# Kernel tuning notes

Measured on AMD Instinct MI355X. Metric: run time of the kernel, lower is better.

The kernel has to match this reference:

```python
import jax, jax.numpy as jnp
import numpy as np

NUM_SPARSE = 26
VOCAB = 100000
EMB = 64
B = 2048
DENSE = 13
NUM_FEA = NUM_SPARSE + 1  # 26 embeddings + bottom-MLP output


def _xavier(key, shape):
    fan_in, fan_out = shape[0], shape[1]
    lim = jnp.sqrt(6.0 / (fan_in + fan_out))
    return jax.random.uniform(key, shape, jnp.float32, -lim, lim)


def setup_inputs() -> dict:
    key = jax.random.key(0)
    ks = jax.random.split(key, 20)
    inp = {
        "dense": jax.random.normal(ks[0], (B, DENSE), jnp.float32),
        "cat_idx": jax.random.randint(ks[1], (B, NUM_SPARSE), 0, VOCAB, jnp.int32),
        # stacked EmbeddingBag tables (all same vocab -> one [26, V, 64] tensor)
        "tables": _xavier(ks[2], (VOCAB, EMB))[None] * jnp.ones((NUM_SPARSE, 1, 1), jnp.float32) * 0
                  + jax.random.normal(ks[3], (NUM_SPARSE, VOCAB, EMB), jnp.float32) * 0.01,
        # bottom MLP: 13 -> 512 -> 256 -> 64
        "bw0": _xavier(ks[4], (DENSE, 512)), "bb0": jnp.zeros((512,), jnp.float32),
        "bw1": _xavier(ks[5], (512, 256)),   "bb1": jnp.zeros((256,), jnp.float32),
        "bw2": _xavier(ks[6], (256, EMB)),   "bb2": jnp.zeros((EMB,), jnp.float32),
        # top MLP: 415 -> 1024 -> 512 -> 256 -> 1
        "tw0": _xavier(ks[7], (EMB + NUM_FEA * (NUM_FEA - 1) // 2, 1024)), "tb0": jnp.zeros((1024,), jnp.float32),
        "tw1": _xavier(ks[8], (1024, 512)),  "tb1": jnp.zeros((512,), jnp.float32),
        "tw2": _xavier(ks[9], (512, 256)),   "tb2": jnp.zeros((256,), jnp.float32),
        "tw3": _xavier(ks[10], (256, 1)),    "tb3": jnp.zeros((1,), jnp.float32),
    }
    return inp


def reference(dense, cat_idx, tables, bw0, bb0, bw1, bb1, bw2, bb2,
              tw0, tb0, tw1, tb1, tw2, tb2, tw3, tb3):
    # bottom MLP on dense features -> [B, EMB]
    h = jax.nn.relu(dense @ bw0 + bb0)
    h = jax.nn.relu(h @ bw1 + bb1)
    bot = jax.nn.relu(h @ bw2 + bb2)

    # EmbeddingBag (single index per bag, sum mode == plain gather): [B, 26, EMB]
    feat_ids = jnp.arange(NUM_SPARSE)[None, :]  # [1, 26]
    emb = tables[feat_ids, cat_idx]             # [B, 26, EMB]

    # dot interaction: batched Gram matrix then lower-triangular gather
    T = jnp.concatenate([bot[:, None, :], emb], axis=1)  # [B, 27, EMB]
    Z = jnp.einsum("bif,bjf->bij", T, T)                  # [B, 27, 27]
    li, lj = np.tril_indices(NUM_FEA, k=-1)               # 351 pairs
    Zflat = Z[:, li, lj]                                  # [B, 351]

    R = jnp.concatenate([bot, Zflat], axis=1)             # [B, 415]

    # top MLP
    r = jax.nn.relu(R @ tw0 + tb0)
    r = jax.nn.relu(r @ tw1 + tb1)
    r = jax.nn.relu(r @ tw2 + tb2)
    out = jax.nn.sigmoid(r @ tw3 + tb3)                   # [B, 1]
    return out
```

## Files before the change

### kernel.cpp

```cpp
#include <hip/hip_runtime.h>
#include <hip/hip_bf16.h>


#define BATCH 2048
#define VOCAB 100000
#define EMB 64
#define NSPARSE 26
#define NFEA 27
#define NPAIR 351
#define RLD 416

typedef __attribute__((ext_vector_type(8))) __bf16 bf16x8;
typedef __attribute__((ext_vector_type(4))) float f32x4;
typedef __hip_bfloat16 bf16;

#define GLOAD16(g, l)                                                          \
    __builtin_amdgcn_global_load_lds(                                          \
        (const __attribute__((address_space(1))) unsigned int*)(g),            \
        (__attribute__((address_space(3))) unsigned int*)(l), 16, 0, 0)

__global__ __launch_bounds__(256) void gemm_bf16(
    const bf16* __restrict__ A,
    const bf16* __restrict__ Wt,
    const float* __restrict__ bias,
    bf16* __restrict__ C,
    int M, int N, int K, int ldC)
{
    __shared__ __align__(16) bf16 As[64 * 32];
    __shared__ __align__(16) bf16 Bs[64 * 32];

    const int t   = threadIdx.x;
    const int nbn = N >> 6;
    const int bm  = blockIdx.x / nbn;
    const int bn  = blockIdx.x % nbn;
    const int row0 = bm << 6, n0 = bn << 6;

    const int wid  = t >> 6, lane = t & 63;
    const int wr   = wid >> 1, wc = wid & 1;
    const int lr   = lane & 15;
    const int q    = lane >> 4;

    const int srow = t >> 2, sslot = t & 3;
    const int sswz = sslot ^ ((srow >> 1) & 3);
    const char* gA = (const char*)(A  + (size_t)(row0 + srow) * K) + sswz * 16;
    const char* gB = (const char*)(Wt + (size_t)(n0   + srow) * K) + sswz * 16;
    char* lA = (char*)As + t * 16;
    char* lB = (char*)Bs + t * 16;

    f32x4 acc[2][2] = {};

    const int arow0 = wr * 32 + lr;
    const int brow0 = wc * 32 + lr;

    for (int k0 = 0; k0 < K; k0 += 32) {
        GLOAD16(gA + (size_t)k0 * 2, lA);
        GLOAD16(gB + (size_t)k0 * 2, lB);
        __syncthreads();

        bf16x8 af[2], bf[2];
#pragma unroll
        for (int m = 0; m < 2; ++m) {
            const int r = arow0 + 16 * m;
            af[m] = *(const bf16x8*)((const char*)As + r * 64 +
                                     ((q ^ ((r >> 1) & 3)) << 4));
        }
#pragma unroll
        for (int n = 0; n < 2; ++n) {
            const int r = brow0 + 16 * n;
            bf[n] = *(const bf16x8*)((const char*)Bs + r * 64 +
                                     ((q ^ ((r >> 1) & 3)) << 4));
        }
#pragma unroll
        for (int m = 0; m < 2; ++m)
#pragma unroll
            for (int n = 0; n < 2; ++n)
                acc[m][n] = __builtin_amdgcn_mfma_f32_16x16x32_bf16(
                    af[m], bf[n], acc[m][n], 0, 0, 0);
        __syncthreads();
    }

#pragma unroll
    for (int n = 0; n < 2; ++n) {
        const int col = n0 + wc * 32 + 16 * n + lr;
        const float bv = bias[col];
#pragma unroll
        for (int m = 0; m < 2; ++m) {
#pragma unroll
            for (int i = 0; i < 4; ++i) {
                const int row = row0 + wr * 32 + 16 * m + q * 4 + i;
                float v = acc[m][n][i] + bv;
                v = fmaxf(v, 0.f);
                C[(size_t)row * ldC + col] = __float2bfloat16(v);
            }
        }
    }
}

struct WConvArgs {
    const float* src[6];
    bf16*        dst[6];
    int K[6], N[6], Kp[6], t0[7];
};

__global__ __launch_bounds__(256) void wconv_kernel(WConvArgs a)
{
    __shared__ float Ts[32][33];
    int w = 0;
    while (w < 5 && (int)blockIdx.x >= a.t0[w + 1]) ++w;
    const int rel = blockIdx.x - a.t0[w];
    const int K = a.K[w], N = a.N[w], Kp = a.Kp[w];
    const int nbn = N >> 5;
    const int tk = rel / nbn, tn = rel % nbn;
    const int tx = threadIdx.x & 31, ty = threadIdx.x >> 5;

    const float* src = a.src[w];
    bf16* dst = a.dst[w];

#pragma unroll
    for (int rr = 0; rr < 4; ++rr) {
        const int k = tk * 32 + ty + rr * 8;
        const int n = tn * 32 + tx;
        Ts[ty + rr * 8][tx] = (k < K) ? src[(size_t)k * N + n] : 0.f;
    }
    __syncthreads();
#pragma unroll
    for (int rr = 0; rr < 4; ++rr) {
        const int n = tn * 32 + ty + rr * 8;
        const int kp = tk * 32 + tx;
        dst[(size_t)n * Kp + kp] = __float2bfloat16(Ts[tx][ty + rr * 8]);
    }
}

__global__ __launch_bounds__(256) void densepad_kernel(
    const float* __restrict__ dense, bf16* __restrict__ out)
{
    const int i = blockIdx.x * 256 + threadIdx.x;
    const int b = i >> 5, c = i & 31;
    out[i] = (c < 13) ? __float2bfloat16(dense[b * 13 + c]) : __float2bfloat16(0.f);
}

__global__ __launch_bounds__(256) void interact_kernel(
    const int* __restrict__ cat_idx, const float* __restrict__ tables,
    bf16* __restrict__ R)
{
    __shared__ float T[NFEA][EMB + 1];

    const int b    = blockIdx.x;
    const int t    = threadIdx.x;
    const int g    = t >> 6;
    const int lane = t & 63;
    bf16* Rrow = R + (size_t)b * RLD;

    for (int f = g; f < NFEA; f += 4) {
        if (f == 0) {
            T[0][lane] = __bfloat162float(Rrow[lane]);
        } else {
            const int j   = f - 1;
            const int idx = cat_idx[b * NSPARSE + j];
            T[f][lane] = tables[((size_t)j * VOCAB + idx) * EMB + lane];
        }
    }
    __syncthreads();

    if (t == 0) Rrow[415] = __float2bfloat16(0.f);

    for (int p = t; p < NPAIR; p += 256) {
        int i = (int)((1.0f + sqrtf(1.0f + 8.0f * (float)p)) * 0.5f);
        while (i * (i - 1) / 2 > p) --i;
        while ((i + 1) * i / 2 <= p) ++i;
        const int j = p - i * (i - 1) / 2;
        float s = 0.f;
#pragma unroll 16
        for (int k = 0; k < EMB; ++k) s += T[i][k] * T[j][k];
        Rrow[EMB + p] = __float2bfloat16(s);
    }
}

__global__ __launch_bounds__(256) void top3_kernel(
    const bf16* __restrict__ A, const float* __restrict__ w,
    const float* __restrict__ bias, float* __restrict__ out)
{
    const int gid  = blockIdx.x * 256 + threadIdx.x;
    const int row  = gid >> 6;
    const int lane = gid & 63;

    const bf16* arow = A + (size_t)row * 256;
    float s = 0.f;
#pragma unroll
    for (int k = lane; k < 256; k += 64)
        s += __bfloat162float(arow[k]) * w[k];
#pragma unroll
    for (int off = 32; off; off >>= 1) s += __shfl_down(s, off);
    if (lane == 0) out[row] = 1.f / (1.f + expf(-(s + bias[0])));
}

extern "C" void kernel_launch(void* const* d_in, const int* in_sizes, int n_in,
                              void* d_out, int out_size, void* d_ws, size_t ws_size,
                              hipStream_t stream)
{
    const float* dense   = (const float*)d_in[0];
    const int*   cat_idx = (const int*)  d_in[1];
    const float* tables  = (const float*)d_in[2];
    const float* bw0 = (const float*)d_in[3];
    const float* bb0 = (const float*)d_in[4];
    const float* bw1 = (const float*)d_in[5];
    const float* bb1 = (const float*)d_in[6];
    const float* bw2 = (const float*)d_in[7];
    const float* bb2 = (const float*)d_in[8];
    const float* tw0 = (const float*)d_in[9];
    const float* tb0 = (const float*)d_in[10];
    const float* tw1 = (const float*)d_in[11];
    const float* tb1 = (const float*)d_in[12];
    const float* tw2 = (const float*)d_in[13];
    const float* tb2 = (const float*)d_in[14];
    const float* tw3 = (const float*)d_in[15];
    const float* tb3 = (const float*)d_in[16];

    bf16* p = (bf16*)d_ws;
    bf16* dense_bf = p; p += (size_t)BATCH * 32;
    bf16* h0   = p; p += (size_t)BATCH * 512;
    bf16* h1   = p; p += (size_t)BATCH * 256;
    bf16* R    = p; p += (size_t)BATCH * RLD;
    bf16* r0   = p; p += (size_t)BATCH * 1024;
    bf16* r1   = p; p += (size_t)BATCH * 512;
    bf16* r2   = p; p += (size_t)BATCH * 256;
    bf16* bw0t = p; p += 512 * 32;
    bf16* bw1t = p; p += 256 * 512;
    bf16* bw2t = p; p += 64 * 256;
    bf16* tw0t = p; p += 1024 * RLD;
    bf16* tw1t = p; p += 512 * 1024;
    bf16* tw2t = p; p += 256 * 512;
    float* out = (float*)d_out;

    WConvArgs wa;
    wa.src[0] = bw0;  wa.dst[0] = bw0t; wa.K[0] = 13;   wa.N[0] = 512;  wa.Kp[0] = 32;
    wa.src[1] = bw1;  wa.dst[1] = bw1t; wa.K[1] = 512;  wa.N[1] = 256;  wa.Kp[1] = 512;
    wa.src[2] = bw2;  wa.dst[2] = bw2t; wa.K[2] = 256;  wa.N[2] = 64;   wa.Kp[2] = 256;
    wa.src[3] = tw0;  wa.dst[3] = tw0t; wa.K[3] = 415;  wa.N[3] = 1024; wa.Kp[3] = RLD;
    wa.src[4] = tw1;  wa.dst[4] = tw1t; wa.K[4] = 1024; wa.N[4] = 512;  wa.Kp[4] = 1024;
    wa.src[5] = tw2;  wa.dst[5] = tw2t; wa.K[5] = 512;  wa.N[5] = 256;  wa.Kp[5] = 512;
    int tiles = 0;
    for (int w = 0; w < 6; ++w) {
        wa.t0[w] = tiles;
        tiles += (wa.Kp[w] >> 5) * (wa.N[w] >> 5);
    }
    wa.t0[6] = tiles;

    wconv_kernel<<<tiles, 256, 0, stream>>>(wa);
    densepad_kernel<<<(BATCH * 32) / 256, 256, 0, stream>>>(dense, dense_bf);

    gemm_bf16<<<(BATCH / 64) * (512 / 64), 256, 0, stream>>>(
        dense_bf, bw0t, bb0, h0, BATCH, 512, 32, 512);
    gemm_bf16<<<(BATCH / 64) * (256 / 64), 256, 0, stream>>>(
        h0, bw1t, bb1, h1, BATCH, 256, 512, 256);
    gemm_bf16<<<(BATCH / 64) * (64 / 64), 256, 0, stream>>>(
        h1, bw2t, bb2, R, BATCH, 64, 256, RLD);

    interact_kernel<<<BATCH, 256, 0, stream>>>(cat_idx, tables, R);

    gemm_bf16<<<(BATCH / 64) * (1024 / 64), 256, 0, stream>>>(
        R, tw0t, tb0, r0, BATCH, 1024, RLD, 1024);
    gemm_bf16<<<(BATCH / 64) * (512 / 64), 256, 0, stream>>>(
        r0, tw1t, tb1, r1, BATCH, 512, 1024, 512);
    gemm_bf16<<<(BATCH / 64) * (256 / 64), 256, 0, stream>>>(
        r1, tw2t, tb2, r2, BATCH, 256, 512, 256);
    top3_kernel<<<BATCH / 4, 256, 0, stream>>>(r2, tw3, tb3, out);
}
```

Before: 72.73 us.

## Fuse entire DLRM forward into one persistent-per-16-rows megakernel

Replaces the chain of densepad, six tiled GEMM launches, the interaction kernel and the final dot kernel with a single kernel where each block owns 16 batch rows and keeps every activation in LDS. Weights are streamed straight from global memory into MFMA operands with no LDS staging. The Gram matrix is now computed with MFMA instead of scalar loops, and the last layer plus sigmoid is folded into the tw2 epilogue. This removes launch overhead and the global round-trips of the intermediate activations. In exchange only 128 blocks run, so each block re-reads all weights from L2, occupancy is low, and the weight loads are not coalesced through shared memory.

New measurement: 120.2 us. 1.65x slower.

```diff
diff --git a/kernel.cpp b/kernel.cpp
--- a/kernel.cpp
+++ b/kernel.cpp
@@ -4,97 +4,12 @@
 
 #define BATCH 2048
 #define VOCAB 100000
-#define EMB 64
-#define NSPARSE 26
-#define NFEA 27
-#define NPAIR 351
-#define RLD 416
 
 typedef __attribute__((ext_vector_type(8))) __bf16 bf16x8;
 typedef __attribute__((ext_vector_type(4))) float f32x4;
 typedef __hip_bfloat16 bf16;
 
-#define GLOAD16(g, l)                                                          \
-    __builtin_amdgcn_global_load_lds(                                          \
-        (const __attribute__((address_space(1))) unsigned int*)(g),            \
-        (__attribute__((address_space(3))) unsigned int*)(l), 16, 0, 0)
-
-__global__ __launch_bounds__(256) void gemm_bf16(
-    const bf16* __restrict__ A,
-    const bf16* __restrict__ Wt,
-    const float* __restrict__ bias,
-    bf16* __restrict__ C,
-    int M, int N, int K, int ldC)
-{
-    __shared__ __align__(16) bf16 As[64 * 32];
-    __shared__ __align__(16) bf16 Bs[64 * 32];
-
-    const int t   = threadIdx.x;
-    const int nbn = N >> 6;
-    const int bm  = blockIdx.x / nbn;
-    const int bn  = blockIdx.x % nbn;
-    const int row0 = bm << 6, n0 = bn << 6;
-
-    const int wid  = t >> 6, lane = t & 63;
-    const int wr   = wid >> 1, wc = wid & 1;
-    const int lr   = lane & 15;
-    const int q    = lane >> 4;
-
-    const int srow = t >> 2, sslot = t & 3;
-    const int sswz = sslot ^ ((srow >> 1) & 3);
-    const char* gA = (const char*)(A  + (size_t)(row0 + srow) * K) + sswz * 16;
-    const char* gB = (const char*)(Wt + (size_t)(n0   + srow) * K) + sswz * 16;
-    char* lA = (char*)As + t * 16;
-    char* lB = (char*)Bs + t * 16;
-
-    f32x4 acc[2][2] = {};
-
-    const int arow0 = wr * 32 + lr;
-    const int brow0 = wc * 32 + lr;
-
-    for (int k0 = 0; k0 < K; k0 += 32) {
-        GLOAD16(gA + (size_t)k0 * 2, lA);
-        GLOAD16(gB + (size_t)k0 * 2, lB);
-        __syncthreads();
-
-        bf16x8 af[2], bf[2];
-#pragma unroll
-        for (int m = 0; m < 2; ++m) {
-            const int r = arow0 + 16 * m;
-            af[m] = *(const bf16x8*)((const char*)As + r * 64 +
-                                     ((q ^ ((r >> 1) & 3)) << 4));
-        }
-#pragma unroll
-        for (int n = 0; n < 2; ++n) {
-            const int r = brow0 + 16 * n;
-            bf[n] = *(const bf16x8*)((const char*)Bs + r * 64 +
-                                     ((q ^ ((r >> 1) & 3)) << 4));
-        }
-#pragma unroll
-        for (int m = 0; m < 2; ++m)
-#pragma unroll
-            for (int n = 0; n < 2; ++n)
-                acc[m][n] = __builtin_amdgcn_mfma_f32_16x16x32_bf16(
-                    af[m], bf[n], acc[m][n], 0, 0, 0);
-        __syncthreads();
-    }
-
-#pragma unroll
-    for (int n = 0; n < 2; ++n) {
-        const int col = n0 + wc * 32 + 16 * n + lr;
-        const float bv = bias[col];
-#pragma unroll
-        for (int m = 0; m < 2; ++m) {
-#pragma unroll
-            for (int i = 0; i < 4; ++i) {
-                const int row = row0 + wr * 32 + 16 * m + q * 4 + i;
-                float v = acc[m][n][i] + bv;
-                v = fmaxf(v, 0.f);
-                C[(size_t)row * ldC + col] = __float2bfloat16(v);
-            }
-        }
-    }
-}
+#define MFMA __builtin_amdgcn_mfma_f32_16x16x32_bf16
 
 struct WConvArgs {
     const float* src[6];
@@ -131,67 +46,194 @@
     }
 }
 
-__global__ __launch_bounds__(256) void densepad_kernel(
-    const float* __restrict__ dense, bf16* __restrict__ out)
-{
-    const int i = blockIdx.x * 256 + threadIdx.x;
-    const int b = i >> 5, c = i & 31;
-    out[i] = (c < 13) ? __float2bfloat16(dense[b * 13 + c]) : __float2bfloat16(0.f);
-}
-
-__global__ __launch_bounds__(256) void interact_kernel(
-    const int* __restrict__ cat_idx, const float* __restrict__ tables,
-    bf16* __restrict__ R)
-{
-    __shared__ float T[NFEA][EMB + 1];
-
-    const int b    = blockIdx.x;
-    const int t    = threadIdx.x;
-    const int g    = t >> 6;
-    const int lane = t & 63;
-    bf16* Rrow = R + (size_t)b * RLD;
-
-    for (int f = g; f < NFEA; f += 4) {
-        if (f == 0) {
-            T[0][lane] = __bfloat162float(Rrow[lane]);
-        } else {
-            const int j   = f - 1;
-            const int idx = cat_idx[b * NSPARSE + j];
-            T[f][lane] = tables[((size_t)j * VOCAB + idx) * EMB + lane];
-        }
-    }
-    __syncthreads();
-
-    if (t == 0) Rrow[415] = __float2bfloat16(0.f);
-
-    for (int p = t; p < NPAIR; p += 256) {
-        int i = (int)((1.0f + sqrtf(1.0f + 8.0f * (float)p)) * 0.5f);
-        while (i * (i - 1) / 2 > p) --i;
-        while ((i + 1) * i / 2 <= p) ++i;
-        const int j = p - i * (i - 1) / 2;
-        float s = 0.f;
-#pragma unroll 16
-        for (int k = 0; k < EMB; ++k) s += T[i][k] * T[j][k];
-        Rrow[EMB + p] = __float2bfloat16(s);
-    }
-}
-
-__global__ __launch_bounds__(256) void top3_kernel(
-    const bf16* __restrict__ A, const float* __restrict__ w,
-    const float* __restrict__ bias, float* __restrict__ out)
-{
-    const int gid  = blockIdx.x * 256 + threadIdx.x;
-    const int row  = gid >> 6;
-    const int lane = gid & 63;
-
-    const bf16* arow = A + (size_t)row * 256;
-    float s = 0.f;
-#pragma unroll
-    for (int k = lane; k < 256; k += 64)
-        s += __bfloat162float(arow[k]) * w[k];
-#pragma unroll
-    for (int off = 32; off; off >>= 1) s += __shfl_down(s, off);
-    if (lane == 0) out[row] = 1.f / (1.f + expf(-(s + bias[0])));
+template<int KSTEPS, int NREP>
+__device__ __forceinline__ void layer(
+    const bf16* actL, int strideA,
+    const bf16* __restrict__ Wt, const float* __restrict__ bias,
+    bf16* outL, int strideO,
+    int wid, int lr, int q)
+{
+    constexpr int K = KSTEPS * 32;
+    const int n0 = wid * NREP * 16;
+
+    const bf16* wp[NREP];
+#pragma unroll
+    for (int n = 0; n < NREP; ++n)
+        wp[n] = Wt + (size_t)(n0 + n * 16 + lr) * K + q * 8;
+    const bf16* ap = actL + lr * strideA + q * 8;
+
+    f32x4 acc[NREP] = {};
+#pragma unroll 4
+    for (int ks = 0; ks < KSTEPS; ++ks) {
+        const bf16x8 af = *(const bf16x8*)(ap + ks * 32);
+#pragma unroll
+        for (int n = 0; n < NREP; ++n) {
+            const bf16x8 bv = *(const bf16x8*)(wp[n] + ks * 32);
+            acc[n] = MFMA(af, bv, acc[n], 0, 0, 0);
+        }
+    }
+
+#pragma unroll
+    for (int n = 0; n < NREP; ++n) {
+        const int col = n0 + n * 16 + lr;
+        const float bv = bias[col];
+#pragma unroll
+        for (int i = 0; i < 4; ++i) {
+            float v = fmaxf(acc[n][i] + bv, 0.f);
+            outL[(q * 4 + i) * strideO + col] = __float2bfloat16(v);
+        }
+    }
+}
+
+__global__ __launch_bounds__(256, 1) void mega(
+    const float* __restrict__ dense, const int* __restrict__ cat,
+    const float* __restrict__ tables,
+    const bf16* __restrict__ bw0t, const float* __restrict__ bb0,
+    const bf16* __restrict__ bw1t, const float* __restrict__ bb1,
+    const bf16* __restrict__ bw2t, const float* __restrict__ bb2,
+    const bf16* __restrict__ tw0t, const float* __restrict__ tb0,
+    const bf16* __restrict__ tw1t, const float* __restrict__ tb1,
+    const bf16* __restrict__ tw2t, const float* __restrict__ tb2,
+    const float* __restrict__ tw3, const float* __restrict__ tb3,
+    float* __restrict__ out)
+{
+    __shared__ __align__(16) bf16 T[16 * 32 * 72];
+    __shared__ __align__(16) bf16 bufA[16 * 264];
+    __shared__ __align__(16) bf16 bufB[16 * 520];
+    __shared__ float rsum[4][16];
+
+    const int t   = threadIdx.x;
+    const int b0  = blockIdx.x * 16;
+    const int wid = t >> 6, lane = t & 63;
+    const int lr  = lane & 15, q = lane >> 4;
+
+    for (int i = t; i < 16 * 32; i += 256) {
+        const int r = i >> 5, c = i & 31;
+        const float v = (c < 13) ? dense[(size_t)(b0 + r) * 13 + c] : 0.f;
+        bufA[r * 40 + c] = __float2bfloat16(v);
+    }
+    __syncthreads();
+
+    layer<1, 8>(bufA, 40, bw0t, bb0, bufB, 520, wid, lr, q);
+    __syncthreads();
+
+    layer<16, 4>(bufB, 520, bw1t, bb1, bufA, 264, wid, lr, q);
+    __syncthreads();
+
+    for (int task = t; task < 416 * 16; task += 256) {
+        const int g = task >> 4, c4 = task & 15;
+        const int r = g / 26, j = g - r * 26;
+        const int idx = cat[(b0 + r) * 26 + j];
+        const float4 v =
+            *(const float4*)&tables[((size_t)j * VOCAB + idx) * 64 + c4 * 4];
+        union { bf16 h[4]; uint2 u; } pk;
+        pk.h[0] = __float2bfloat16(v.x); pk.h[1] = __float2bfloat16(v.y);
+        pk.h[2] = __float2bfloat16(v.z); pk.h[3] = __float2bfloat16(v.w);
+        *(uint2*)&T[(r * 32 + 1 + j) * 72 + c4 * 4] = pk.u;
+    }
+
+    layer<8, 1>(bufA, 264, bw2t, bb2, T, 32 * 72, wid, lr, q);
+
+    for (int i = t; i < 16 * 33; i += 256) {
+        const int r = i / 33, c = i % 33;
+        bufB[r * 456 + 415 + c] = __float2bfloat16(0.f);
+    }
+    __syncthreads();
+
+    for (int i = t; i < 16 * 64; i += 256) {
+        const int r = i >> 6, c = i & 63;
+        bufB[r * 456 + c] = T[r * (32 * 72) + c];
+    }
+
+    {
+#pragma unroll
+        for (int rr = 0; rr < 4; ++rr) {
+            const int r = wid * 4 + rr;
+            const bf16* Tr = T + r * (32 * 72);
+            f32x4 g00 = {}, g10 = {}, g11 = {};
+#pragma unroll
+            for (int ks = 0; ks < 2; ++ks) {
+                const bf16x8 a0 = *(const bf16x8*)(Tr + lr * 72 + ks * 32 + q * 8);
+                const bf16x8 a1 = *(const bf16x8*)(Tr + (16 + lr) * 72 + ks * 32 + q * 8);
+                g00 = MFMA(a0, a0, g00, 0, 0, 0);
+                g10 = MFMA(a1, a0, g10, 0, 0, 0);
+                g11 = MFMA(a1, a1, g11, 0, 0, 0);
+            }
+#pragma unroll
+            for (int i = 0; i < 4; ++i) {
+                {   const int row = q * 4 + i, col = lr;
+                    if (col < row) {
+                        const int p = row * (row - 1) / 2 + col;
+                        bufB[r * 456 + 64 + p] = __float2bfloat16(g00[i]);
+                    } }
+                {   const int row = 16 + q * 4 + i, col = lr;
+                    if (row < 27) {
+                        const int p = row * (row - 1) / 2 + col;
+                        bufB[r * 456 + 64 + p] = __float2bfloat16(g10[i]);
+                    } }
+                {   const int row = 16 + q * 4 + i, col = 16 + lr;
+                    if (row < 27 && col < row) {
+                        const int p = row * (row - 1) / 2 + col;
+                        bufB[r * 456 + 64 + p] = __float2bfloat16(g11[i]);
+                    } }
+            }
+        }
+    }
+    __syncthreads();
+
+    bf16* r0 = T;
+    layer<14, 16>(bufB, 456, tw0t, tb0, r0, 1032, wid, lr, q);
+    __syncthreads();
+
+    layer<32, 8>(r0, 1032, tw1t, tb1, bufB, 520, wid, lr, q);
+    __syncthreads();
+
+    {
+        constexpr int KST = 16, NR = 4;
+        constexpr int K = 512;
+        const int n0 = wid * 64;
+        const bf16* wp[NR];
+#pragma unroll
+        for (int n = 0; n < NR; ++n)
+            wp[n] = tw2t + (size_t)(n0 + n * 16 + lr) * K + q * 8;
+        const bf16* ap = bufB + lr * 520 + q * 8;
+
+        f32x4 acc[NR] = {};
+#pragma unroll 4
+        for (int ks = 0; ks < KST; ++ks) {
+            const bf16x8 af = *(const bf16x8*)(ap + ks * 32);
+#pragma unroll
+            for (int n = 0; n < NR; ++n)
+                acc[n] = MFMA(af, *(const bf16x8*)(wp[n] + ks * 32), acc[n], 0, 0, 0);
+        }
+
+        float s[4] = {0.f, 0.f, 0.f, 0.f};
+#pragma unroll
+        for (int n = 0; n < NR; ++n) {
+            const int col = n0 + n * 16 + lr;
+            const float bv = tb2[col];
+            const float wv = tw3[col];
+#pragma unroll
+            for (int i = 0; i < 4; ++i)
+                s[i] += fmaxf(acc[n][i] + bv, 0.f) * wv;
+        }
+#pragma unroll
+        for (int i = 0; i < 4; ++i) {
+            s[i] += __shfl_xor(s[i], 1);
+            s[i] += __shfl_xor(s[i], 2);
+            s[i] += __shfl_xor(s[i], 4);
+            s[i] += __shfl_xor(s[i], 8);
+        }
+        if (lr == 0) {
+#pragma unroll
+            for (int i = 0; i < 4; ++i) rsum[wid][q * 4 + i] = s[i];
+        }
+        __syncthreads();
+        if (t < 16) {
+            const float tot = rsum[0][t] + rsum[1][t] + rsum[2][t] + rsum[3][t];
+            out[b0 + t] = 1.f / (1.f + expf(-(tot + tb3[0])));
+        }
+    }
 }
 
 extern "C" void kernel_launch(void* const* d_in, const int* in_sizes, int n_in,
@@ -217,17 +259,10 @@
     const float* tb3 = (const float*)d_in[16];
 
     bf16* p = (bf16*)d_ws;
-    bf16* dense_bf = p; p += (size_t)BATCH * 32;
-    bf16* h0   = p; p += (size_t)BATCH * 512;
-    bf16* h1   = p; p += (size_t)BATCH * 256;
-    bf16* R    = p; p += (size_t)BATCH * RLD;
-    bf16* r0   = p; p += (size_t)BATCH * 1024;
-    bf16* r1   = p; p += (size_t)BATCH * 512;
-    bf16* r2   = p; p += (size_t)BATCH * 256;
     bf16* bw0t = p; p += 512 * 32;
     bf16* bw1t = p; p += 256 * 512;
     bf16* bw2t = p; p += 64 * 256;
-    bf16* tw0t = p; p += 1024 * RLD;
+    bf16* tw0t = p; p += 1024 * 448;
     bf16* tw1t = p; p += 512 * 1024;
     bf16* tw2t = p; p += 256 * 512;
     float* out = (float*)d_out;
@@ -236,7 +271,7 @@
     wa.src[0] = bw0;  wa.dst[0] = bw0t; wa.K[0] = 13;   wa.N[0] = 512;  wa.Kp[0] = 32;
     wa.src[1] = bw1;  wa.dst[1] = bw1t; wa.K[1] = 512;  wa.N[1] = 256;  wa.Kp[1] = 512;
     wa.src[2] = bw2;  wa.dst[2] = bw2t; wa.K[2] = 256;  wa.N[2] = 64;   wa.Kp[2] = 256;
-    wa.src[3] = tw0;  wa.dst[3] = tw0t; wa.K[3] = 415;  wa.N[3] = 1024; wa.Kp[3] = RLD;
+    wa.src[3] = tw0;  wa.dst[3] = tw0t; wa.K[3] = 415;  wa.N[3] = 1024; wa.Kp[3] = 448;
     wa.src[4] = tw1;  wa.dst[4] = tw1t; wa.K[4] = 1024; wa.N[4] = 512;  wa.Kp[4] = 1024;
     wa.src[5] = tw2;  wa.dst[5] = tw2t; wa.K[5] = 512;  wa.N[5] = 256;  wa.Kp[5] = 512;
     int tiles = 0;
@@ -247,22 +282,9 @@
     wa.t0[6] = tiles;
 
     wconv_kernel<<<tiles, 256, 0, stream>>>(wa);
-    densepad_kernel<<<(BATCH * 32) / 256, 256, 0, stream>>>(dense, dense_bf);
-
-    gemm_bf16<<<(BATCH / 64) * (512 / 64), 256, 0, stream>>>(
-        dense_bf, bw0t, bb0, h0, BATCH, 512, 32, 512);
-    gemm_bf16<<<(BATCH / 64) * (256 / 64), 256, 0, stream>>>(
-        h0, bw1t, bb1, h1, BATCH, 256, 512, 256);
-    gemm_bf16<<<(BATCH / 64) * (64 / 64), 256, 0, stream>>>(
-        h1, bw2t, bb2, R, BATCH, 64, 256, RLD);
-
-    interact_kernel<<<BATCH, 256, 0, stream>>>(cat_idx, tables, R);
-
-    gemm_bf16<<<(BATCH / 64) * (1024 / 64), 256, 0, stream>>>(
-        R, tw0t, tb0, r0, BATCH, 1024, RLD, 1024);
-    gemm_bf16<<<(BATCH / 64) * (512 / 64), 256, 0, stream>>>(
-        r0, tw1t, tb1, r1, BATCH, 512, 1024, 512);
-    gemm_bf16<<<(BATCH / 64) * (256 / 64), 256, 0, stream>>>(
-        r1, tw2t, tb2, r2, BATCH, 256, 512, 256);
-    top3_kernel<<<BATCH / 4, 256, 0, stream>>>(r2, tw3, tb3, out);
-}
+
+    mega<<<BATCH / 16, 256, 0, stream>>>(
+        dense, cat_idx, tables,
+        bw0t, bb0, bw1t, bb1, bw2t, bb2,
+        tw0t, tb0, tw1t, tb1, tw2t, tb2, tw3, tb3, out);
+}
```
